# Kernel tuning notes

Measured on AMD Instinct MI355X. Metric: run time of the kernel, lower is better.

Reference implementation:

```python
import jax, jax.numpy as jnp
import numpy as np

DIM_Q = 512
DIM_K = 512
DIM_V = 512
NUM_HEADS = 8
LN_EPS = 1e-5


def setup_inputs() -> dict:
    key = jax.random.key(0)
    ks = jax.random.split(key, 12)
    s_q = 1.0 / np.sqrt(DIM_Q)
    s_k = 1.0 / np.sqrt(DIM_K)
    s_v = 1.0 / np.sqrt(DIM_V)
    return {
        "Q": jax.random.normal(ks[0], (8, 1024, DIM_Q), dtype=jnp.float32),
        "K": jax.random.normal(ks[1], (8, 1024, DIM_K), dtype=jnp.float32),
        "Wq": jax.random.uniform(ks[2], (DIM_Q, DIM_V), jnp.float32, -s_q, s_q),
        "bq": jax.random.uniform(ks[3], (DIM_V,), jnp.float32, -s_q, s_q),
        "Wk": jax.random.uniform(ks[4], (DIM_K, DIM_V), jnp.float32, -s_k, s_k),
        "bk": jax.random.uniform(ks[5], (DIM_V,), jnp.float32, -s_k, s_k),
        "Wv": jax.random.uniform(ks[6], (DIM_K, DIM_V), jnp.float32, -s_k, s_k),
        "bv": jax.random.uniform(ks[7], (DIM_V,), jnp.float32, -s_k, s_k),
        "Wo": jax.random.uniform(ks[8], (DIM_V, DIM_V), jnp.float32, -s_v, s_v),
        "bo": jax.random.uniform(ks[9], (DIM_V,), jnp.float32, -s_v, s_v),
        "g0": jnp.ones((DIM_V,), jnp.float32),
        "b0": jnp.zeros((DIM_V,), jnp.float32),
        "g1": jnp.ones((DIM_V,), jnp.float32),
        "b1": jnp.zeros((DIM_V,), jnp.float32),
    }


def _layer_norm(x, gamma, beta):
    mu = jnp.mean(x, axis=-1, keepdims=True)
    var = jnp.var(x, axis=-1, keepdims=True)
    return (x - mu) * jax.lax.rsqrt(var + LN_EPS) * gamma + beta


def reference(Q, K, Wq, bq, Wk, bk, Wv, bv, Wo, bo, g0, b0, g1, b1):
    B, Nq, _ = Q.shape
    Nk = K.shape[1]
    H = NUM_HEADS
    d = DIM_V // H  # head dim

    Qp = Q @ Wq + bq                      # [B, Nq, dim_V]
    Kp = K @ Wk + bk                      # [B, Nk, dim_V]
    Vp = K @ Wv + bv                      # [B, Nk, dim_V]

    Qh = Qp.reshape(B, Nq, H, d)
    Kh = Kp.reshape(B, Nk, H, d)
    Vh = Vp.reshape(B, Nk, H, d)

    scores = jnp.einsum("bqhd,bkhd->bhqk", Qh, Kh) / jnp.sqrt(jnp.float32(d))
    A = jax.nn.softmax(scores, axis=-1)   # [B, H, Nq, Nk]
    Oh = jnp.einsum("bhqk,bkhd->bqhd", A, Vh) + Qh  # residual with projected Q
    O = Oh.reshape(B, Nq, DIM_V)

    O = _layer_norm(O, g0, b0)
    O = O + jax.nn.relu(O @ Wo + bo)
    O = _layer_norm(O, g1, b1)
    return O
```

## Files before the change

kernel.cpp:

```cpp
#include <hip/hip_runtime.h>
#include <math.h>

#define DV 512
#define HD 64
#define NHEADS 8
#define SEQ 1024
#define NBATCH 8
#define MROWS (NBATCH * SEQ)

typedef __bf16 bf16;
typedef __bf16 bf16x8 __attribute__((ext_vector_type(8)));
typedef __bf16 bf16x4 __attribute__((ext_vector_type(4)));
typedef __bf16 bf16x2 __attribute__((ext_vector_type(2)));
typedef float f32x4 __attribute__((ext_vector_type(4)));

__device__ inline void gload_lds16(const void* g, void* l) {
  __builtin_amdgcn_global_load_lds(
      (const __attribute__((address_space(1))) unsigned int*)g,
      (__attribute__((address_space(3))) unsigned int*)l, 16, 0, 0);
}

__global__ __launch_bounds__(256) void cast_f32_bf16(
    const float* __restrict__ s0, const float* __restrict__ s1,
    bf16* __restrict__ d0, bf16* __restrict__ d1)
{
  const float* src = blockIdx.z ? s1 : s0;
  bf16* dst = blockIdx.z ? d1 : d0;
  int i = blockIdx.x * 256 + threadIdx.x;
  const float4* s = (const float4*)src;
  float4 a = s[i * 2], b = s[i * 2 + 1];
  bf16x8 o;
  o[0] = (bf16)a.x; o[1] = (bf16)a.y; o[2] = (bf16)a.z; o[3] = (bf16)a.w;
  o[4] = (bf16)b.x; o[5] = (bf16)b.y; o[6] = (bf16)b.z; o[7] = (bf16)b.w;
  *(bf16x8*)(dst + (size_t)i * 8) = o;
}

__global__ __launch_bounds__(256) void transpose_cast_w(
    const float* __restrict__ W0, const float* __restrict__ W1,
    const float* __restrict__ W2, const float* __restrict__ W3,
    bf16* __restrict__ T0, bf16* __restrict__ T1,
    bf16* __restrict__ T2, bf16* __restrict__ T3)
{
  const float* W = blockIdx.z == 0 ? W0 : blockIdx.z == 1 ? W1 : blockIdx.z == 2 ? W2 : W3;
  bf16* WT = blockIdx.z == 0 ? T0 : blockIdx.z == 1 ? T1 : blockIdx.z == 2 ? T2 : T3;
  __shared__ float T[64][65];
  const int t = threadIdx.x;
  const int k0 = blockIdx.y * 64, n0 = blockIdx.x * 64;
#pragma unroll
  for (int p = 0; p < 4; ++p) {
    int r = p * 16 + (t >> 4), c = (t & 15) * 4;
    float4 v = *(const float4*)&W[(size_t)(k0 + r) * DV + n0 + c];
    T[r][c] = v.x; T[r][c + 1] = v.y; T[r][c + 2] = v.z; T[r][c + 3] = v.w;
  }
  __syncthreads();
#pragma unroll
  for (int p = 0; p < 2; ++p) {
    int n = p * 32 + (t >> 3), kc = (t & 7) * 8;
    bf16x8 o;
#pragma unroll
    for (int j = 0; j < 8; ++j) o[j] = (bf16)T[kc + j][n];
    *(bf16x8*)&WT[(size_t)(n0 + n) * DV + k0 + kc] = o;
  }
}

__device__ __forceinline__ void gemm_core128(
    const bf16* __restrict__ A, const bf16* __restrict__ B,
    bf16* As, bf16* Bs, int m0, int n0, int Kd, f32x4 (*acc)[4])
{
  const int tid = threadIdx.x;
  const int lane = tid & 63, w = tid >> 6;
  const int wm = w >> 1, wn = w & 1;
  const int cl = lane & 15, qd = lane >> 4;

  for (int k0 = 0; k0 < Kd; k0 += 64) {
    __syncthreads();
#pragma unroll
    for (int t = 0; t < 4; ++t) {
      int S = t * 256 + tid;
      int row = S >> 3, kq = (S & 7) ^ (row & 7);
      gload_lds16(A + (size_t)(m0 + row) * Kd + k0 + kq * 8,
                  As + (size_t)(t * 256 + w * 64) * 8);
    }
#pragma unroll
    for (int t = 0; t < 4; ++t) {
      int S = t * 256 + tid;
      int row = S >> 3, kq = (S & 7) ^ (row & 7);
      gload_lds16(B + (size_t)(n0 + row) * Kd + k0 + kq * 8,
                  Bs + (size_t)(t * 256 + w * 64) * 8);
    }
    __syncthreads();

#pragma unroll
    for (int cc = 0; cc < 2; ++cc) {
      bf16x8 af[4], bfr[4];
#pragma unroll
      for (int mi = 0; mi < 4; ++mi) {
        int row = wm * 64 + mi * 16 + cl;
        int slot = row * 8 + ((cc * 4 + qd) ^ (row & 7));
        af[mi] = *(const bf16x8*)(As + (size_t)slot * 8);
      }
#pragma unroll
      for (int ni = 0; ni < 4; ++ni) {
        int row = wn * 64 + ni * 16 + cl;
        int slot = row * 8 + ((cc * 4 + qd) ^ (row & 7));
        bfr[ni] = *(const bf16x8*)(Bs + (size_t)slot * 8);
      }
#pragma unroll
      for (int mi = 0; mi < 4; ++mi)
#pragma unroll
        for (int ni = 0; ni < 4; ++ni)
          acc[mi][ni] = __builtin_amdgcn_mfma_f32_16x16x32_bf16(
              af[mi], bfr[ni], acc[mi][ni], 0, 0, 0);
    }
  }
}

__global__ __launch_bounds__(256) void gemm_proj(
    const bf16* __restrict__ A0, const bf16* __restrict__ A1, const bf16* __restrict__ A2,
    const bf16* __restrict__ B0, const bf16* __restrict__ B1, const bf16* __restrict__ B2,
    const float* __restrict__ c0, const float* __restrict__ c1, const float* __restrict__ c2,
    bf16* __restrict__ O0, bf16* __restrict__ O1, bf16* __restrict__ O2)
{
  __shared__ bf16 As[128 * 64];
  __shared__ bf16 Bs[128 * 64];
  const int z = blockIdx.z;
  const bf16* A = z == 0 ? A0 : z == 1 ? A1 : A2;
  const bf16* B = z == 0 ? B0 : z == 1 ? B1 : B2;
  const float* bias = z == 0 ? c0 : z == 1 ? c1 : c2;
  bf16* C = z == 0 ? O0 : z == 1 ? O1 : O2;
  const int N = (z == 2) ? MROWS : DV;
  int bx, by;
  if (z < 2) { bx = blockIdx.x & 3;  by = blockIdx.x >> 2; }
  else       { bx = blockIdx.x & 63; by = blockIdx.x >> 6; }
  const int m0 = by * 128, n0 = bx * 128;

  f32x4 acc[4][4] = {};
  gemm_core128(A, B, As, Bs, m0, n0, DV, acc);

  const int lane = threadIdx.x & 63, w = threadIdx.x >> 6;
  const int wm = w >> 1, wn = w & 1;
  const int cl = lane & 15, qd = lane >> 4;
  float bcol[4] = {0.f, 0.f, 0.f, 0.f};
  if (z < 2)
#pragma unroll
    for (int ni = 0; ni < 4; ++ni) bcol[ni] = bias[n0 + wn * 64 + ni * 16 + cl];
#pragma unroll
  for (int mi = 0; mi < 4; ++mi)
#pragma unroll
    for (int r = 0; r < 4; ++r) {
      int gm = m0 + wm * 64 + mi * 16 + qd * 4 + r;
      float brow = (z == 2) ? bias[gm] : 0.f;
#pragma unroll
      for (int ni = 0; ni < 4; ++ni) {
        int gn = n0 + wn * 64 + ni * 16 + cl;
        float v = acc[mi][ni][r] + (z == 2 ? brow : bcol[ni]);
        C[(size_t)gm * N + gn] = (bf16)v;
      }
    }
}

__global__ __launch_bounds__(256) void gemm_out(
    const bf16* __restrict__ A, const bf16* __restrict__ B,
    const float* __restrict__ bias, const bf16* __restrict__ res,
    float* __restrict__ Cout)
{
  __shared__ bf16 As[128 * 64];
  __shared__ bf16 Bs[64 * 64];
  const int tid = threadIdx.x;
  const int lane = tid & 63, w = tid >> 6;
  const int wm = w >> 1, wn = w & 1;
  const int cl = lane & 15, qd = lane >> 4;
  const int m0 = blockIdx.y * 128, n0 = blockIdx.x * 64;

  f32x4 acc[4][2] = {};
  for (int k0 = 0; k0 < DV; k0 += 64) {
    __syncthreads();
#pragma unroll
    for (int t = 0; t < 4; ++t) {
      int S = t * 256 + tid;
      int row = S >> 3, kq = (S & 7) ^ (row & 7);
      gload_lds16(A + (size_t)(m0 + row) * DV + k0 + kq * 8,
                  As + (size_t)(t * 256 + w * 64) * 8);
    }
#pragma unroll
    for (int t = 0; t < 2; ++t) {
      int S = t * 256 + tid;
      int row = S >> 3, kq = (S & 7) ^ (row & 7);
      gload_lds16(B + (size_t)(n0 + row) * DV + k0 + kq * 8,
                  Bs + (size_t)(t * 256 + w * 64) * 8);
    }
    __syncthreads();
#pragma unroll
    for (int cc = 0; cc < 2; ++cc) {
      bf16x8 af[4], bfr[2];
#pragma unroll
      for (int mi = 0; mi < 4; ++mi) {
        int row = wm * 64 + mi * 16 + cl;
        int slot = row * 8 + ((cc * 4 + qd) ^ (row & 7));
        af[mi] = *(const bf16x8*)(As + (size_t)slot * 8);
      }
#pragma unroll
      for (int ni = 0; ni < 2; ++ni) {
        int row = wn * 32 + ni * 16 + cl;
        int slot = row * 8 + ((cc * 4 + qd) ^ (row & 7));
        bfr[ni] = *(const bf16x8*)(Bs + (size_t)slot * 8);
      }
#pragma unroll
      for (int mi = 0; mi < 4; ++mi)
#pragma unroll
        for (int ni = 0; ni < 2; ++ni)
          acc[mi][ni] = __builtin_amdgcn_mfma_f32_16x16x32_bf16(
              af[mi], bfr[ni], acc[mi][ni], 0, 0, 0);
    }
  }

  float bcol[2] = { bias[n0 + wn * 32 + cl], bias[n0 + wn * 32 + 16 + cl] };
#pragma unroll
  for (int mi = 0; mi < 4; ++mi)
#pragma unroll
    for (int r = 0; r < 4; ++r) {
      int gm = m0 + wm * 64 + mi * 16 + qd * 4 + r;
#pragma unroll
      for (int ni = 0; ni < 2; ++ni) {
        int gn = n0 + wn * 32 + ni * 16 + cl;
        size_t off = (size_t)gm * DV + gn;
        float v = acc[mi][ni][r] + bcol[ni];
        Cout[off] = (float)res[off] + fmaxf(v, 0.f);
      }
    }
}

__global__ __launch_bounds__(256) void attn_mfma(
    const bf16* __restrict__ Qp, const bf16* __restrict__ Kp,
    const bf16* __restrict__ VpT, float* __restrict__ O)
{
  __shared__ bf16 Ks[2][64 * 64];
  __shared__ bf16 Vs[2][64 * 64];
  __shared__ bf16 Ps[4][32 * 72];

  const int tid = threadIdx.x, lane = tid & 63, w = tid >> 6;
  const int cl = lane & 15, qd = lane >> 4;
  const int bh = blockIdx.y, b = bh >> 3, h = bh & 7;
  const int q0w = blockIdx.x * 128 + w * 32;

  const float SCL = 0.18033688011112042f;
  bf16x8 qa[2][2];
#pragma unroll
  for (int qt = 0; qt < 2; ++qt)
#pragma unroll
    for (int ch = 0; ch < 2; ++ch) {
      bf16x8 v = *(const bf16x8*)(Qp + ((size_t)b * SEQ + q0w + qt * 16 + cl) * DV
                                  + h * HD + ch * 32 + qd * 8);
#pragma unroll
      for (int j = 0; j < 8; ++j) v[j] = (bf16)((float)v[j] * SCL);
      qa[qt][ch] = v;
    }

  f32x4 o[4][2] = {};
  float lrun[2] = {0.f, 0.f};

  const bf16* Kbase = Kp + (size_t)b * SEQ * DV + h * HD;
  const bf16* Vbase = VpT + (size_t)h * HD * MROWS + (size_t)b * SEQ;
  bf16* Pw = &Ps[w][0];

  const int Sa = tid, Sb = 256 + tid;
  const int kRowA = Sa >> 3, kDgA = (Sa & 7) ^ (kRowA & 7);
  const int kRowB = Sb >> 3, kDgB = (Sb & 7) ^ (kRowB & 7);
  const size_t kOffA = (size_t)kRowA * DV + kDgA * 8;
  const size_t kOffB = (size_t)kRowB * DV + kDgB * 8;
  const size_t vOffA = (size_t)kRowA * MROWS + kDgA * 8;
  const size_t vOffB = (size_t)kRowB * MROWS + kDgB * 8;

  {
    gload_lds16(Kbase + kOffA, &Ks[0][(size_t)(w * 64) * 8]);
    gload_lds16(Kbase + kOffB, &Ks[0][(size_t)(256 + w * 64) * 8]);
    gload_lds16(Vbase + vOffA, &Vs[0][(size_t)(w * 64) * 8]);
    gload_lds16(Vbase + vOffB, &Vs[0][(size_t)(256 + w * 64) * 8]);
  }

  for (int it = 0; it < SEQ / 64; ++it) {
    __syncthreads();
    const int cur = it & 1;
    if (it + 1 < SEQ / 64) {
      const size_t kt = (size_t)(it + 1) * 64;
      gload_lds16(Kbase + kt * DV + kOffA, &Ks[cur ^ 1][(size_t)(w * 64) * 8]);
      gload_lds16(Kbase + kt * DV + kOffB, &Ks[cur ^ 1][(size_t)(256 + w * 64) * 8]);
      gload_lds16(Vbase + kt + vOffA, &Vs[cur ^ 1][(size_t)(w * 64) * 8]);
      gload_lds16(Vbase + kt + vOffB, &Vs[cur ^ 1][(size_t)(256 + w * 64) * 8]);
    }
    const bf16* K_ = &Ks[cur][0];
    const bf16* V_ = &Vs[cur][0];

    f32x4 sc[4][2] = {};
#pragma unroll
    for (int ch = 0; ch < 2; ++ch) {
      bf16x8 kf[4];
#pragma unroll
      for (int kt4 = 0; kt4 < 4; ++kt4) {
        int key = kt4 * 16 + cl;
        int slot = key * 8 + ((ch * 4 + qd) ^ (key & 7));
        kf[kt4] = *(const bf16x8*)(K_ + (size_t)slot * 8);
      }
#pragma unroll
      for (int kt4 = 0; kt4 < 4; ++kt4)
#pragma unroll
        for (int qt = 0; qt < 2; ++qt)
          sc[kt4][qt] = __builtin_amdgcn_mfma_f32_16x16x32_bf16(
              kf[kt4], qa[qt][ch], sc[kt4][qt], 0, 0, 0);
    }

#pragma unroll
    for (int qt = 0; qt < 2; ++qt) {
      float sum = 0.f;
#pragma unroll
      for (int kt4 = 0; kt4 < 4; ++kt4) {
        float p0 = __builtin_amdgcn_exp2f(sc[kt4][qt][0]);
        float p1 = __builtin_amdgcn_exp2f(sc[kt4][qt][1]);
        float p2 = __builtin_amdgcn_exp2f(sc[kt4][qt][2]);
        float p3 = __builtin_amdgcn_exp2f(sc[kt4][qt][3]);
        sum += (p0 + p1) + (p2 + p3);
        bf16x4 pk;
        pk[0] = (bf16)p0; pk[1] = (bf16)p1; pk[2] = (bf16)p2; pk[3] = (bf16)p3;
        *(bf16x4*)(Pw + (size_t)(qt * 16 + cl) * 72 + kt4 * 16 + qd * 4) = pk;
      }
      sum += __shfl_xor(sum, 16);
      sum += __shfl_xor(sum, 32);
      lrun[qt] += sum;
    }

#pragma unroll
    for (int kc = 0; kc < 2; ++kc) {
      bf16x8 pb[2];
#pragma unroll
      for (int qt = 0; qt < 2; ++qt)
        pb[qt] = *(const bf16x8*)(Pw + (size_t)(qt * 16 + cl) * 72 + kc * 32 + qd * 8);
#pragma unroll
      for (int dt = 0; dt < 4; ++dt) {
        int d = dt * 16 + cl;
        int slot = d * 8 + ((kc * 4 + qd) ^ (d & 7));
        bf16x8 vf = *(const bf16x8*)(V_ + (size_t)slot * 8);
#pragma unroll
        for (int qt = 0; qt < 2; ++qt)
          o[dt][qt] = __builtin_amdgcn_mfma_f32_16x16x32_bf16(
              vf, pb[qt], o[dt][qt], 0, 0, 0);
      }
    }
  }

#pragma unroll
  for (int qt = 0; qt < 2; ++qt) {
    float inv = 1.f / lrun[qt];
    size_t rowoff = ((size_t)b * SEQ + q0w + qt * 16 + cl) * DV + h * HD;
#pragma unroll
    for (int dt = 0; dt < 4; ++dt) {
      float4 st;
      st.x = o[dt][qt][0] * inv; st.y = o[dt][qt][1] * inv;
      st.z = o[dt][qt][2] * inv; st.w = o[dt][qt][3] * inv;
      *(float4*)&O[rowoff + dt * 16 + qd * 4] = st;
    }
  }
}

__global__ __launch_bounds__(256) void ln_res_bf16(
    const float* __restrict__ X, const bf16* __restrict__ Rq,
    const float* __restrict__ g, const float* __restrict__ be,
    bf16* __restrict__ Y)
{
  const int row = blockIdx.x * 4 + (threadIdx.x >> 6);
  const int l = threadIdx.x & 63;
  const float* x = X + (size_t)row * DV + l * 8;
  float4 a = ((const float4*)x)[0], c = ((const float4*)x)[1];
  bf16x8 rv = *(const bf16x8*)(Rq + (size_t)row * DV + l * 8);
  a.x += (float)rv[0]; a.y += (float)rv[1]; a.z += (float)rv[2]; a.w += (float)rv[3];
  c.x += (float)rv[4]; c.y += (float)rv[5]; c.z += (float)rv[6]; c.w += (float)rv[7];
  float s  = (a.x + a.y) + (a.z + a.w) + (c.x + c.y) + (c.z + c.w);
  float s2 = a.x*a.x + a.y*a.y + a.z*a.z + a.w*a.w + c.x*c.x + c.y*c.y + c.z*c.z + c.w*c.w;
#pragma unroll
  for (int off = 1; off < 64; off <<= 1) {
    s += __shfl_xor(s, off);
    s2 += __shfl_xor(s2, off);
  }
  float mu = s * (1.f / DV);
  float var = s2 * (1.f / DV) - mu * mu;
  float inv = rsqrtf(var + 1e-5f);
  float4 g1 = ((const float4*)(g + l * 8))[0], g2 = ((const float4*)(g + l * 8))[1];
  float4 b1 = ((const float4*)(be + l * 8))[0], b2 = ((const float4*)(be + l * 8))[1];
  bf16x8 ov;
  ov[0] = (bf16)((a.x - mu) * inv * g1.x + b1.x);
  ov[1] = (bf16)((a.y - mu) * inv * g1.y + b1.y);
  ov[2] = (bf16)((a.z - mu) * inv * g1.z + b1.z);
  ov[3] = (bf16)((a.w - mu) * inv * g1.w + b1.w);
  ov[4] = (bf16)((c.x - mu) * inv * g2.x + b2.x);
  ov[5] = (bf16)((c.y - mu) * inv * g2.y + b2.y);
  ov[6] = (bf16)((c.z - mu) * inv * g2.z + b2.z);
  ov[7] = (bf16)((c.w - mu) * inv * g2.w + b2.w);
  *(bf16x8*)(Y + (size_t)row * DV + l * 8) = ov;
}

__global__ __launch_bounds__(256) void ln_inplace(
    float* __restrict__ X, const float* __restrict__ g, const float* __restrict__ be)
{
  const int row = blockIdx.x * 4 + (threadIdx.x >> 6);
  const int l = threadIdx.x & 63;
  float* x = X + (size_t)row * DV + l * 8;
  float4 a = ((const float4*)x)[0], c = ((const float4*)x)[1];
  float s  = (a.x + a.y) + (a.z + a.w) + (c.x + c.y) + (c.z + c.w);
  float s2 = a.x*a.x + a.y*a.y + a.z*a.z + a.w*a.w + c.x*c.x + c.y*c.y + c.z*c.z + c.w*c.w;
#pragma unroll
  for (int off = 1; off < 64; off <<= 1) {
    s += __shfl_xor(s, off);
    s2 += __shfl_xor(s2, off);
  }
  float mu = s * (1.f / DV);
  float var = s2 * (1.f / DV) - mu * mu;
  float inv = rsqrtf(var + 1e-5f);
  float4 g1 = ((const float4*)(g + l * 8))[0], g2 = ((const float4*)(g + l * 8))[1];
  float4 b1 = ((const float4*)(be + l * 8))[0], b2 = ((const float4*)(be + l * 8))[1];
  a.x = (a.x - mu) * inv * g1.x + b1.x;
  a.y = (a.y - mu) * inv * g1.y + b1.y;
  a.z = (a.z - mu) * inv * g1.z + b1.z;
  a.w = (a.w - mu) * inv * g1.w + b1.w;
  c.x = (c.x - mu) * inv * g2.x + b2.x;
  c.y = (c.y - mu) * inv * g2.y + b2.y;
  c.z = (c.z - mu) * inv * g2.z + b2.z;
  c.w = (c.w - mu) * inv * g2.w + b2.w;
  ((float4*)x)[0] = a;
  ((float4*)x)[1] = c;
}

extern "C" void kernel_launch(void* const* d_in, const int* in_sizes, int n_in,
                              void* d_out, int out_size, void* d_ws, size_t ws_size,
                              hipStream_t stream)
{
  const float* Q  = (const float*)d_in[0];
  const float* Kf = (const float*)d_in[1];
  const float* Wq = (const float*)d_in[2];
  const float* bq = (const float*)d_in[3];
  const float* Wk = (const float*)d_in[4];
  const float* bk = (const float*)d_in[5];
  const float* Wv = (const float*)d_in[6];
  const float* bv = (const float*)d_in[7];
  const float* Wo = (const float*)d_in[8];
  const float* bo = (const float*)d_in[9];
  const float* g0 = (const float*)d_in[10];
  const float* b0 = (const float*)d_in[11];
  const float* g1 = (const float*)d_in[12];
  const float* b1 = (const float*)d_in[13];
  float* out = (float*)d_out;

  const size_t MB = 1ull << 20;
  char* W = (char*)d_ws;
  bf16* Qb  = (bf16*)(W + 0);
  bf16* Kb  = (bf16*)(W + 8 * MB);
  bf16* Qp  = (bf16*)(W + 16 * MB);
  bf16* Kp  = (bf16*)(W + 24 * MB);
  bf16* VpT = (bf16*)(W + 32 * MB);
  bf16* WqT = (bf16*)(W + 40 * MB);
  bf16* WkT = (bf16*)(W + 40 * MB + 512 * 1024);
  bf16* WvT = (bf16*)(W + 41 * MB);
  bf16* WoT = (bf16*)(W + 41 * MB + 512 * 1024);
  bf16* Xb  = (bf16*)(W + 42 * MB);
  float* Ob = (float*)(W + 0);

  dim3 blk(256);
  cast_f32_bf16<<<dim3(2048, 1, 2), blk, 0, stream>>>(Q, Kf, Qb, Kb);
  transpose_cast_w<<<dim3(8, 8, 4), blk, 0, stream>>>(Wq, Wk, Wv, Wo, WqT, WkT, WvT, WoT);
  gemm_proj<<<dim3(256, 1, 3), blk, 0, stream>>>(
      Qb, Kb, WvT, WqT, WkT, Kb, bq, bk, bv, Qp, Kp, VpT);
  attn_mfma<<<dim3(SEQ / 128, NBATCH * NHEADS), blk, 0, stream>>>(Qp, Kp, VpT, Ob);
  ln_res_bf16<<<dim3(MROWS / 4), blk, 0, stream>>>(Ob, Qp, g0, b0, Xb);
  gemm_out<<<dim3(DV / 64, MROWS / 128), blk, 0, stream>>>(Xb, WoT, bo, Xb, out);
  ln_inplace<<<dim3(MROWS / 4), blk, 0, stream>>>(out, g1, b1);
}
```

Measured before the change: 194.9 us.

## Double-buffer GEMM LDS loads, fuse residual into attention, merge prep kernels

Both GEMM kernels now double-buffer their LDS tiles and prefetch the next K-slice while the current one is being multiplied, with one barrier per iteration instead of two. The attention kernel adds the projected-Q residual itself and writes bf16 instead of fp32, so the first layernorm reads half the bytes and skips the separate residual load. The input cast and weight transpose kernels are merged into one launch, saving a launch at the cost of many idle blocks in the weight slices. The risks are a larger LDS footprint that may lower occupancy, and bf16 rounding of the pre-layernorm activations.

```diff
diff --git a/kernel.cpp b/kernel.cpp
--- a/kernel.cpp
+++ b/kernel.cpp
@@ -11,7 +11,6 @@
 typedef __bf16 bf16;
 typedef __bf16 bf16x8 __attribute__((ext_vector_type(8)));
 typedef __bf16 bf16x4 __attribute__((ext_vector_type(4)));
-typedef __bf16 bf16x2 __attribute__((ext_vector_type(2)));
 typedef float f32x4 __attribute__((ext_vector_type(4)));
 
 __device__ inline void gload_lds16(const void* g, void* l) {
@@ -20,32 +19,33 @@
       (__attribute__((address_space(3))) unsigned int*)l, 16, 0, 0);
 }
 
-__global__ __launch_bounds__(256) void cast_f32_bf16(
-    const float* __restrict__ s0, const float* __restrict__ s1,
-    bf16* __restrict__ d0, bf16* __restrict__ d1)
-{
-  const float* src = blockIdx.z ? s1 : s0;
-  bf16* dst = blockIdx.z ? d1 : d0;
-  int i = blockIdx.x * 256 + threadIdx.x;
-  const float4* s = (const float4*)src;
-  float4 a = s[i * 2], b = s[i * 2 + 1];
-  bf16x8 o;
-  o[0] = (bf16)a.x; o[1] = (bf16)a.y; o[2] = (bf16)a.z; o[3] = (bf16)a.w;
-  o[4] = (bf16)b.x; o[5] = (bf16)b.y; o[6] = (bf16)b.z; o[7] = (bf16)b.w;
-  *(bf16x8*)(dst + (size_t)i * 8) = o;
-}
-
-__global__ __launch_bounds__(256) void transpose_cast_w(
+__global__ __launch_bounds__(256) void prep_kernel(
+    const float* __restrict__ Qf, const float* __restrict__ Kf,
+    bf16* __restrict__ Qb, bf16* __restrict__ Kb,
     const float* __restrict__ W0, const float* __restrict__ W1,
     const float* __restrict__ W2, const float* __restrict__ W3,
     bf16* __restrict__ T0, bf16* __restrict__ T1,
     bf16* __restrict__ T2, bf16* __restrict__ T3)
 {
-  const float* W = blockIdx.z == 0 ? W0 : blockIdx.z == 1 ? W1 : blockIdx.z == 2 ? W2 : W3;
-  bf16* WT = blockIdx.z == 0 ? T0 : blockIdx.z == 1 ? T1 : blockIdx.z == 2 ? T2 : T3;
+  const int z = blockIdx.z;
+  if (z < 2) {
+    const float* src = z ? Kf : Qf;
+    bf16* dst = z ? Kb : Qb;
+    int i = blockIdx.x * 256 + threadIdx.x;
+    const float4* s = (const float4*)src;
+    float4 a = s[i * 2], b = s[i * 2 + 1];
+    bf16x8 o;
+    o[0] = (bf16)a.x; o[1] = (bf16)a.y; o[2] = (bf16)a.z; o[3] = (bf16)a.w;
+    o[4] = (bf16)b.x; o[5] = (bf16)b.y; o[6] = (bf16)b.z; o[7] = (bf16)b.w;
+    *(bf16x8*)(dst + (size_t)i * 8) = o;
+    return;
+  }
+  if (blockIdx.x >= 64) return;
+  const float* W = z == 2 ? W0 : z == 3 ? W1 : z == 4 ? W2 : W3;
+  bf16* WT = z == 2 ? T0 : z == 3 ? T1 : z == 4 ? T2 : T3;
   __shared__ float T[64][65];
   const int t = threadIdx.x;
-  const int k0 = blockIdx.y * 64, n0 = blockIdx.x * 64;
+  const int k0 = (blockIdx.x >> 3) * 64, n0 = (blockIdx.x & 7) * 64;
 #pragma unroll
   for (int p = 0; p < 4; ++p) {
     int r = p * 16 + (t >> 4), c = (t & 15) * 4;
@@ -63,7 +63,7 @@
   }
 }
 
-__device__ __forceinline__ void gemm_core128(
+__device__ __forceinline__ void gemm_core128_db(
     const bf16* __restrict__ A, const bf16* __restrict__ B,
     bf16* As, bf16* Bs, int m0, int n0, int Kd, f32x4 (*acc)[4])
 {
@@ -72,24 +72,38 @@
   const int wm = w >> 1, wn = w & 1;
   const int cl = lane & 15, qd = lane >> 4;
 
-  for (int k0 = 0; k0 < Kd; k0 += 64) {
+  size_t offA[4], offB[4];
+  int ldsOff[4];
+#pragma unroll
+  for (int t = 0; t < 4; ++t) {
+    int S = t * 256 + tid;
+    int row = S >> 3, kq = (S & 7) ^ (row & 7);
+    offA[t] = (size_t)(m0 + row) * Kd + kq * 8;
+    offB[t] = (size_t)(n0 + row) * Kd + kq * 8;
+    ldsOff[t] = (t * 256 + w * 64) * 8;
+  }
+
+#pragma unroll
+  for (int t = 0; t < 4; ++t) {
+    gload_lds16(A + offA[t], As + ldsOff[t]);
+    gload_lds16(B + offB[t], Bs + ldsOff[t]);
+  }
+
+  const int nIter = Kd >> 6;
+  for (int it = 0; it < nIter; ++it) {
     __syncthreads();
-#pragma unroll
-    for (int t = 0; t < 4; ++t) {
-      int S = t * 256 + tid;
-      int row = S >> 3, kq = (S & 7) ^ (row & 7);
-      gload_lds16(A + (size_t)(m0 + row) * Kd + k0 + kq * 8,
-                  As + (size_t)(t * 256 + w * 64) * 8);
-    }
-#pragma unroll
-    for (int t = 0; t < 4; ++t) {
-      int S = t * 256 + tid;
-      int row = S >> 3, kq = (S & 7) ^ (row & 7);
-      gload_lds16(B + (size_t)(n0 + row) * Kd + k0 + kq * 8,
-                  Bs + (size_t)(t * 256 + w * 64) * 8);
-    }
-    __syncthreads();
-
+    const int cur = it & 1;
+    if (it + 1 < nIter) {
+      const size_t k0n = (size_t)(it + 1) * 64;
+      const int nb = (cur ^ 1) * 8192;
+#pragma unroll
+      for (int t = 0; t < 4; ++t) {
+        gload_lds16(A + k0n + offA[t], As + nb + ldsOff[t]);
+        gload_lds16(B + k0n + offB[t], Bs + nb + ldsOff[t]);
+      }
+    }
+    const bf16* A_ = As + cur * 8192;
+    const bf16* B_ = Bs + cur * 8192;
 #pragma unroll
     for (int cc = 0; cc < 2; ++cc) {
       bf16x8 af[4], bfr[4];
@@ -97,13 +111,13 @@
       for (int mi = 0; mi < 4; ++mi) {
         int row = wm * 64 + mi * 16 + cl;
         int slot = row * 8 + ((cc * 4 + qd) ^ (row & 7));
-        af[mi] = *(const bf16x8*)(As + (size_t)slot * 8);
+        af[mi] = *(const bf16x8*)(A_ + (size_t)slot * 8);
       }
 #pragma unroll
       for (int ni = 0; ni < 4; ++ni) {
         int row = wn * 64 + ni * 16 + cl;
         int slot = row * 8 + ((cc * 4 + qd) ^ (row & 7));
-        bfr[ni] = *(const bf16x8*)(Bs + (size_t)slot * 8);
+        bfr[ni] = *(const bf16x8*)(B_ + (size_t)slot * 8);
       }
 #pragma unroll
       for (int mi = 0; mi < 4; ++mi)
@@ -121,8 +135,8 @@
     const float* __restrict__ c0, const float* __restrict__ c1, const float* __restrict__ c2,
     bf16* __restrict__ O0, bf16* __restrict__ O1, bf16* __restrict__ O2)
 {
-  __shared__ bf16 As[128 * 64];
-  __shared__ bf16 Bs[128 * 64];
+  __shared__ bf16 As[2 * 128 * 64];
+  __shared__ bf16 Bs[2 * 128 * 64];
   const int z = blockIdx.z;
   const bf16* A = z == 0 ? A0 : z == 1 ? A1 : A2;
   const bf16* B = z == 0 ? B0 : z == 1 ? B1 : B2;
@@ -135,7 +149,7 @@
   const int m0 = by * 128, n0 = bx * 128;
 
   f32x4 acc[4][4] = {};
-  gemm_core128(A, B, As, Bs, m0, n0, DV, acc);
+  gemm_core128_db(A, B, As, Bs, m0, n0, DV, acc);
 
   const int lane = threadIdx.x & 63, w = threadIdx.x >> 6;
   const int wm = w >> 1, wn = w & 1;
@@ -164,32 +178,51 @@
     const float* __restrict__ bias, const bf16* __restrict__ res,
     float* __restrict__ Cout)
 {
-  __shared__ bf16 As[128 * 64];
-  __shared__ bf16 Bs[64 * 64];
+  __shared__ bf16 As[2 * 128 * 64];
+  __shared__ bf16 Bs[2 * 64 * 64];
   const int tid = threadIdx.x;
   const int lane = tid & 63, w = tid >> 6;
   const int wm = w >> 1, wn = w & 1;
   const int cl = lane & 15, qd = lane >> 4;
   const int m0 = blockIdx.y * 128, n0 = blockIdx.x * 64;
 
+  size_t offA[4], offB[2];
+  int ldsA[4], ldsB[2];
+#pragma unroll
+  for (int t = 0; t < 4; ++t) {
+    int S = t * 256 + tid;
+    int row = S >> 3, kq = (S & 7) ^ (row & 7);
+    offA[t] = (size_t)(m0 + row) * DV + kq * 8;
+    ldsA[t] = (t * 256 + w * 64) * 8;
+  }
+#pragma unroll
+  for (int t = 0; t < 2; ++t) {
+    int S = t * 256 + tid;
+    int row = S >> 3, kq = (S & 7) ^ (row & 7);
+    offB[t] = (size_t)(n0 + row) * DV + kq * 8;
+    ldsB[t] = (t * 256 + w * 64) * 8;
+  }
+
+#pragma unroll
+  for (int t = 0; t < 4; ++t) gload_lds16(A + offA[t], As + ldsA[t]);
+#pragma unroll
+  for (int t = 0; t < 2; ++t) gload_lds16(B + offB[t], Bs + ldsB[t]);
+
   f32x4 acc[4][2] = {};
-  for (int k0 = 0; k0 < DV; k0 += 64) {
+  for (int it = 0; it < DV / 64; ++it) {
     __syncthreads();
-#pragma unroll
-    for (int t = 0; t < 4; ++t) {
-      int S = t * 256 + tid;
-      int row = S >> 3, kq = (S & 7) ^ (row & 7);
-      gload_lds16(A + (size_t)(m0 + row) * DV + k0 + kq * 8,
-                  As + (size_t)(t * 256 + w * 64) * 8);
-    }
-#pragma unroll
-    for (int t = 0; t < 2; ++t) {
-      int S = t * 256 + tid;
-      int row = S >> 3, kq = (S & 7) ^ (row & 7);
-      gload_lds16(B + (size_t)(n0 + row) * DV + k0 + kq * 8,
-                  Bs + (size_t)(t * 256 + w * 64) * 8);
-    }
-    __syncthreads();
+    const int cur = it & 1;
+    if (it + 1 < DV / 64) {
+      const size_t k0n = (size_t)(it + 1) * 64;
+#pragma unroll
+      for (int t = 0; t < 4; ++t)
+        gload_lds16(A + k0n + offA[t], As + (cur ^ 1) * 8192 + ldsA[t]);
+#pragma unroll
+      for (int t = 0; t < 2; ++t)
+        gload_lds16(B + k0n + offB[t], Bs + (cur ^ 1) * 4096 + ldsB[t]);
+    }
+    const bf16* A_ = As + cur * 8192;
+    const bf16* B_ = Bs + cur * 4096;
 #pragma unroll
     for (int cc = 0; cc < 2; ++cc) {
       bf16x8 af[4], bfr[2];
@@ -197,13 +230,13 @@
       for (int mi = 0; mi < 4; ++mi) {
         int row = wm * 64 + mi * 16 + cl;
         int slot = row * 8 + ((cc * 4 + qd) ^ (row & 7));
-        af[mi] = *(const bf16x8*)(As + (size_t)slot * 8);
+        af[mi] = *(const bf16x8*)(A_ + (size_t)slot * 8);
       }
 #pragma unroll
       for (int ni = 0; ni < 2; ++ni) {
         int row = wn * 32 + ni * 16 + cl;
         int slot = row * 8 + ((cc * 4 + qd) ^ (row & 7));
-        bfr[ni] = *(const bf16x8*)(Bs + (size_t)slot * 8);
+        bfr[ni] = *(const bf16x8*)(B_ + (size_t)slot * 8);
       }
 #pragma unroll
       for (int mi = 0; mi < 4; ++mi)
@@ -232,7 +265,7 @@
 
 __global__ __launch_bounds__(256) void attn_mfma(
     const bf16* __restrict__ Qp, const bf16* __restrict__ Kp,
-    const bf16* __restrict__ VpT, float* __restrict__ O)
+    const bf16* __restrict__ VpT, bf16* __restrict__ Orb)
 {
   __shared__ bf16 Ks[2][64 * 64];
   __shared__ bf16 Vs[2][64 * 64];
@@ -271,12 +304,10 @@
   const size_t vOffA = (size_t)kRowA * MROWS + kDgA * 8;
   const size_t vOffB = (size_t)kRowB * MROWS + kDgB * 8;
 
-  {
-    gload_lds16(Kbase + kOffA, &Ks[0][(size_t)(w * 64) * 8]);
-    gload_lds16(Kbase + kOffB, &Ks[0][(size_t)(256 + w * 64) * 8]);
-    gload_lds16(Vbase + vOffA, &Vs[0][(size_t)(w * 64) * 8]);
-    gload_lds16(Vbase + vOffB, &Vs[0][(size_t)(256 + w * 64) * 8]);
-  }
+  gload_lds16(Kbase + kOffA, &Ks[0][(size_t)(w * 64) * 8]);
+  gload_lds16(Kbase + kOffB, &Ks[0][(size_t)(256 + w * 64) * 8]);
+  gload_lds16(Vbase + vOffA, &Vs[0][(size_t)(w * 64) * 8]);
+  gload_lds16(Vbase + vOffB, &Vs[0][(size_t)(256 + w * 64) * 8]);
 
   for (int it = 0; it < SEQ / 64; ++it) {
     __syncthreads();
@@ -353,28 +384,30 @@
     size_t rowoff = ((size_t)b * SEQ + q0w + qt * 16 + cl) * DV + h * HD;
 #pragma unroll
     for (int dt = 0; dt < 4; ++dt) {
-      float4 st;
-      st.x = o[dt][qt][0] * inv; st.y = o[dt][qt][1] * inv;
-      st.z = o[dt][qt][2] * inv; st.w = o[dt][qt][3] * inv;
-      *(float4*)&O[rowoff + dt * 16 + qd * 4] = st;
-    }
-  }
-}
-
-__global__ __launch_bounds__(256) void ln_res_bf16(
-    const float* __restrict__ X, const bf16* __restrict__ Rq,
-    const float* __restrict__ g, const float* __restrict__ be,
-    bf16* __restrict__ Y)
+      bf16x4 rv = *(const bf16x4*)(Qp + rowoff + dt * 16 + qd * 4);
+      bf16x4 st;
+      st[0] = (bf16)(o[dt][qt][0] * inv + (float)rv[0]);
+      st[1] = (bf16)(o[dt][qt][1] * inv + (float)rv[1]);
+      st[2] = (bf16)(o[dt][qt][2] * inv + (float)rv[2]);
+      st[3] = (bf16)(o[dt][qt][3] * inv + (float)rv[3]);
+      *(bf16x4*)(Orb + rowoff + dt * 16 + qd * 4) = st;
+    }
+  }
+}
+
+__global__ __launch_bounds__(256) void ln_bf16(
+    const bf16* __restrict__ X, const float* __restrict__ g,
+    const float* __restrict__ be, bf16* __restrict__ Y)
 {
   const int row = blockIdx.x * 4 + (threadIdx.x >> 6);
   const int l = threadIdx.x & 63;
-  const float* x = X + (size_t)row * DV + l * 8;
-  float4 a = ((const float4*)x)[0], c = ((const float4*)x)[1];
-  bf16x8 rv = *(const bf16x8*)(Rq + (size_t)row * DV + l * 8);
-  a.x += (float)rv[0]; a.y += (float)rv[1]; a.z += (float)rv[2]; a.w += (float)rv[3];
-  c.x += (float)rv[4]; c.y += (float)rv[5]; c.z += (float)rv[6]; c.w += (float)rv[7];
-  float s  = (a.x + a.y) + (a.z + a.w) + (c.x + c.y) + (c.z + c.w);
-  float s2 = a.x*a.x + a.y*a.y + a.z*a.z + a.w*a.w + c.x*c.x + c.y*c.y + c.z*c.z + c.w*c.w;
+  bf16x8 xv = *(const bf16x8*)(X + (size_t)row * DV + l * 8);
+  float x[8];
+#pragma unroll
+  for (int j = 0; j < 8; ++j) x[j] = (float)xv[j];
+  float s = 0.f, s2 = 0.f;
+#pragma unroll
+  for (int j = 0; j < 8; ++j) { s += x[j]; s2 += x[j] * x[j]; }
 #pragma unroll
   for (int off = 1; off < 64; off <<= 1) {
     s += __shfl_xor(s, off);
@@ -386,14 +419,14 @@
   float4 g1 = ((const float4*)(g + l * 8))[0], g2 = ((const float4*)(g + l * 8))[1];
   float4 b1 = ((const float4*)(be + l * 8))[0], b2 = ((const float4*)(be + l * 8))[1];
   bf16x8 ov;
-  ov[0] = (bf16)((a.x - mu) * inv * g1.x + b1.x);
-  ov[1] = (bf16)((a.y - mu) * inv * g1.y + b1.y);
-  ov[2] = (bf16)((a.z - mu) * inv * g1.z + b1.z);
-  ov[3] = (bf16)((a.w - mu) * inv * g1.w + b1.w);
-  ov[4] = (bf16)((c.x - mu) * inv * g2.x + b2.x);
-  ov[5] = (bf16)((c.y - mu) * inv * g2.y + b2.y);
-  ov[6] = (bf16)((c.z - mu) * inv * g2.z + b2.z);
-  ov[7] = (bf16)((c.w - mu) * inv * g2.w + b2.w);
+  ov[0] = (bf16)((x[0] - mu) * inv * g1.x + b1.x);
+  ov[1] = (bf16)((x[1] - mu) * inv * g1.y + b1.y);
+  ov[2] = (bf16)((x[2] - mu) * inv * g1.z + b1.z);
+  ov[3] = (bf16)((x[3] - mu) * inv * g1.w + b1.w);
+  ov[4] = (bf16)((x[4] - mu) * inv * g2.x + b2.x);
+  ov[5] = (bf16)((x[5] - mu) * inv * g2.y + b2.y);
+  ov[6] = (bf16)((x[6] - mu) * inv * g2.z + b2.z);
+  ov[7] = (bf16)((x[7] - mu) * inv * g2.w + b2.w);
   *(bf16x8*)(Y + (size_t)row * DV + l * 8) = ov;
 }
 
@@ -460,15 +493,15 @@
   bf16* WvT = (bf16*)(W + 41 * MB);
   bf16* WoT = (bf16*)(W + 41 * MB + 512 * 1024);
   bf16* Xb  = (bf16*)(W + 42 * MB);
-  float* Ob = (float*)(W + 0);
+  bf16* Orb = (bf16*)(W + 0);
 
   dim3 blk(256);
-  cast_f32_bf16<<<dim3(2048, 1, 2), blk, 0, stream>>>(Q, Kf, Qb, Kb);
-  transpose_cast_w<<<dim3(8, 8, 4), blk, 0, stream>>>(Wq, Wk, Wv, Wo, WqT, WkT, WvT, WoT);
+  prep_kernel<<<dim3(2048, 1, 6), blk, 0, stream>>>(
+      Q, Kf, Qb, Kb, Wq, Wk, Wv, Wo, WqT, WkT, WvT, WoT);
   gemm_proj<<<dim3(256, 1, 3), blk, 0, stream>>>(
       Qb, Kb, WvT, WqT, WkT, Kb, bq, bk, bv, Qp, Kp, VpT);
-  attn_mfma<<<dim3(SEQ / 128, NBATCH * NHEADS), blk, 0, stream>>>(Qp, Kp, VpT, Ob);
-  ln_res_bf16<<<dim3(MROWS / 4), blk, 0, stream>>>(Ob, Qp, g0, b0, Xb);
+  attn_mfma<<<dim3(SEQ / 128, NBATCH * NHEADS), blk, 0, stream>>>(Qp, Kp, VpT, Orb);
+  ln_bf16<<<dim3(MROWS / 4), blk, 0, stream>>>(Orb, g0, b0, Xb);
   gemm_out<<<dim3(DV / 64, MROWS / 128), blk, 0, stream>>>(Xb, WoT, bo, Xb, out);
   ln_inplace<<<dim3(MROWS / 4), blk, 0, stream>>>(out, g1, b1);
 }
```

Result: faster. 190.8 us (-2.1%).
